# Optimization experiments

Measured on AMD Instinct MI355X. Metric: run time of the kernel, lower is better.

## Reference

```python
import jax, jax.numpy as jnp
import numpy as np
import math

B, S, D = 2, 2048, 1024
H = 16
HD = D // H
SPARSITY = 0.8


def setup_inputs() -> dict:
    key = jax.random.key(0)
    ks = jax.random.split(key, 5)
    scale = 1.0 / math.sqrt(D)
    return {
        "hidden_states": jax.random.normal(ks[0], (B, S, D), dtype=jnp.float32),
        "Wq": jax.random.normal(ks[1], (D, D), dtype=jnp.float32) * scale,
        "bq": jnp.zeros((D,), dtype=jnp.float32),
        "Wk": jax.random.normal(ks[2], (D, D), dtype=jnp.float32) * scale,
        "bk": jnp.zeros((D,), dtype=jnp.float32),
        "Wv": jax.random.normal(ks[3], (D, D), dtype=jnp.float32) * scale,
        "bv": jnp.zeros((D,), dtype=jnp.float32),
        "Wo": jax.random.normal(ks[4], (D, D), dtype=jnp.float32) * scale,
        "bo": jnp.zeros((D,), dtype=jnp.float32),
    }


def reference(hidden_states, Wq, bq, Wk, bk, Wv, bv, Wo, bo):
    b, s, d = hidden_states.shape
    # projections (torch Linear: x @ W.T + b), split heads -> [b, h, s, hd]
    def proj(W, bias):
        y = hidden_states @ W.T + bias
        return y.reshape(b, s, H, HD).transpose(0, 2, 1, 3)

    q = proj(Wq, bq)
    k = proj(Wk, bk)
    v = proj(Wv, bv)

    # scaled dot-product scores [b, h, s, s]
    attn = jnp.einsum("bhqd,bhkd->bhqk", q, k) / math.sqrt(HD)

    # top-k threshold per query row (k-th largest == sort-descending[k-1])
    kk = max(int(s * (1.0 - SPARSITY)), 1)
    thr = jax.lax.top_k(attn, kk)[0][..., kk - 1:kk]  # [b, h, s, 1]
    attn = attn + jnp.where(attn < thr, jnp.float32(-10000.0), jnp.float32(0.0))

    attn = jax.nn.softmax(attn, axis=-1)
    out = jnp.einsum("bhqk,bhkd->bhqd", attn, v)  # [b, h, s, hd]
    out = out.transpose(0, 2, 1, 3).reshape(b, s, d)
    return out @ Wo.T + bo
```

## Files before the change

### kernel.cpp

```cpp
#include <hip/hip_runtime.h>
#include <math.h>

#define S_LEN 2048
#define NH 16
#define HDIM 64
#define BATCH 2
#define BHC 32
#define KK 409
#define DMODEL 1024

typedef __attribute__((ext_vector_type(8))) short bf16x8;
typedef __attribute__((ext_vector_type(4))) float f32x4;

#define SC_STR 1032
#define P_STR  2056
#define T_STR  40

__device__ __forceinline__ unsigned f2ord(float f) {
    unsigned u = __float_as_uint(f);
    return (u & 0x80000000u) ? ~u : (u | 0x80000000u);
}
__device__ __forceinline__ float ord2f(unsigned v) {
    unsigned u = (v & 0x80000000u) ? (v & 0x7fffffffu) : ~v;
    return __uint_as_float(u);
}
__device__ __forceinline__ unsigned short f2bf(float f) {
    unsigned u = __float_as_uint(f);
    u += 0x7fffu + ((u >> 16) & 1u);
    return (unsigned short)(u >> 16);
}
__device__ __forceinline__ float bf2f(unsigned short h) {
    return __uint_as_float(((unsigned)h) << 16);
}

__global__ __launch_bounds__(256)
void split32(const float* __restrict__ in, unsigned short* __restrict__ hi,
             unsigned short* __restrict__ lo, int n4)
{
    const int i = blockIdx.x * 256 + threadIdx.x;
    if (i < n4) {
        const float4 v = ((const float4*)in)[i];
        ushort4 h, l;
        h.x = f2bf(v.x); l.x = f2bf(v.x - bf2f(h.x));
        h.y = f2bf(v.y); l.y = f2bf(v.y - bf2f(h.y));
        h.z = f2bf(v.z); l.z = f2bf(v.z - bf2f(h.z));
        h.w = f2bf(v.w); l.w = f2bf(v.w - bf2f(h.w));
        ((ushort4*)hi)[i] = h;
        ((ushort4*)lo)[i] = l;
    }
}

__global__ __launch_bounds__(256)
void gemm_mfma(const unsigned short* __restrict__ Ah, const unsigned short* __restrict__ Al,
               const unsigned short* __restrict__ Bh, const unsigned short* __restrict__ Bl,
               const float* __restrict__ bias, void* __restrict__ out0,
               void* __restrict__ out1, int mode)
{
    __shared__ __align__(16) unsigned short sAh[128 * T_STR];
    __shared__ __align__(16) unsigned short sAl[128 * T_STR];
    __shared__ __align__(16) unsigned short sBh[64 * T_STR];
    __shared__ __align__(16) unsigned short sBl[64 * T_STR];

    const int tid  = threadIdx.x;
    const int lane = tid & 63;
    const int w    = tid >> 6;
    const int q15  = lane & 15;
    const int quad = lane >> 4;
    const int n0b = blockIdx.x * 64;
    const int m0b = blockIdx.y * 128;
    const int wm = (w >> 1) * 64;
    const int wn = (w & 1) * 32;

    const int ar0 = tid >> 2, aks0 = (tid & 3) * 8;
    const int ar1 = (tid + 256) >> 2, aks1 = aks0;
    const int br = tid >> 2, bks = (tid & 3) * 8;

    const unsigned short* gAh0 = Ah + (size_t)(m0b + ar0) * 1024 + aks0;
    const unsigned short* gAh1 = Ah + (size_t)(m0b + ar1) * 1024 + aks1;
    const unsigned short* gAl0 = Al + (size_t)(m0b + ar0) * 1024 + aks0;
    const unsigned short* gAl1 = Al + (size_t)(m0b + ar1) * 1024 + aks1;
    const unsigned short* gBh = Bh + (size_t)(n0b + br) * 1024 + bks;
    const unsigned short* gBl = Bl + (size_t)(n0b + br) * 1024 + bks;

    f32x4 acc[4][2];
#pragma unroll
    for (int mt = 0; mt < 4; ++mt)
#pragma unroll
        for (int nt = 0; nt < 2; ++nt) acc[mt][nt] = (f32x4){0.f, 0.f, 0.f, 0.f};

#pragma unroll 1
    for (int k0 = 0; k0 < 1024; k0 += 32) {
        const bf16x8 vah0 = *(const bf16x8*)(gAh0 + k0);
        const bf16x8 vah1 = *(const bf16x8*)(gAh1 + k0);
        const bf16x8 val0 = *(const bf16x8*)(gAl0 + k0);
        const bf16x8 val1 = *(const bf16x8*)(gAl1 + k0);
        const bf16x8 vbh  = *(const bf16x8*)(gBh + k0);
        const bf16x8 vbl  = *(const bf16x8*)(gBl + k0);
        __syncthreads();
        *(bf16x8*)(sAh + ar0 * T_STR + aks0) = vah0;
        *(bf16x8*)(sAh + ar1 * T_STR + aks1) = vah1;
        *(bf16x8*)(sAl + ar0 * T_STR + aks0) = val0;
        *(bf16x8*)(sAl + ar1 * T_STR + aks1) = val1;
        *(bf16x8*)(sBh + br * T_STR + bks) = vbh;
        *(bf16x8*)(sBl + br * T_STR + bks) = vbl;
        __syncthreads();

        bf16x8 fbh[2], fbl[2];
#pragma unroll
        for (int nt = 0; nt < 2; ++nt) {
            fbh[nt] = *(const bf16x8*)(sBh + (wn + nt * 16 + q15) * T_STR + quad * 8);
            fbl[nt] = *(const bf16x8*)(sBl + (wn + nt * 16 + q15) * T_STR + quad * 8);
        }
#pragma unroll
        for (int mt = 0; mt < 4; ++mt) {
            const bf16x8 fah = *(const bf16x8*)(sAh + (wm + mt * 16 + q15) * T_STR + quad * 8);
            const bf16x8 fal = *(const bf16x8*)(sAl + (wm + mt * 16 + q15) * T_STR + quad * 8);
#pragma unroll
            for (int nt = 0; nt < 2; ++nt) {
                acc[mt][nt] = __builtin_amdgcn_mfma_f32_16x16x32_bf16(fah, fbh[nt], acc[mt][nt], 0, 0, 0);
                acc[mt][nt] = __builtin_amdgcn_mfma_f32_16x16x32_bf16(fah, fbl[nt], acc[mt][nt], 0, 0, 0);
                acc[mt][nt] = __builtin_amdgcn_mfma_f32_16x16x32_bf16(fal, fbh[nt], acc[mt][nt], 0, 0, 0);
            }
        }
    }

#pragma unroll
    for (int nt = 0; nt < 2; ++nt) {
        const int n = n0b + wn + nt * 16 + q15;
        const float bv = bias[n];
#pragma unroll
        for (int mt = 0; mt < 4; ++mt) {
            const int mb = m0b + wm + mt * 16 + quad * 4;
#pragma unroll
            for (int rg = 0; rg < 4; ++rg) {
                const int m = mb + rg;
                const float o = acc[mt][nt][rg] + bv;
                if (mode == 0) {
                    ((float*)out0)[(size_t)m * 1024 + n] = o;
                } else {
                    const int b = m >> 11, s = m & 2047;
                    const int h = n >> 6, hd = n & 63;
                    const size_t base = ((size_t)((b * NH + h) * S_LEN + s)) * HDIM + hd;
                    if (mode == 3) {
                        ((unsigned short*)out0)[base] = f2bf(o);
                    } else {
                        const unsigned short oh = f2bf(o);
                        ((unsigned short*)out0)[base] = oh;
                        ((unsigned short*)out1)[base] = f2bf(o - bf2f(oh));
                    }
                }
            }
        }
    }
}

__global__ __launch_bounds__(256)
void transpose_v16(const unsigned short* __restrict__ V, unsigned short* __restrict__ Vt)
{
    __shared__ unsigned short t[64][72];
    const int tid = threadIdx.x;
    const int s0 = blockIdx.x * 64;
    const int bh = blockIdx.y;
    const unsigned short* Vb = V + (size_t)bh * S_LEN * HDIM;
#pragma unroll
    for (int i = 0; i < 4; ++i) {
        const int f = tid + i * 256;
        const int s = f >> 4;
        const int hq = (f & 15) * 4;
        const ushort4 v = *(const ushort4*)(Vb + (size_t)(s0 + s) * HDIM + hq);
        t[s][hq + 0] = v.x; t[s][hq + 1] = v.y; t[s][hq + 2] = v.z; t[s][hq + 3] = v.w;
    }
    __syncthreads();
    unsigned short* Vtb = Vt + (size_t)bh * HDIM * S_LEN;
#pragma unroll
    for (int i = 0; i < 4; ++i) {
        const int f = tid + i * 256;
        const int hd = f >> 4;
        const int sq = (f & 15) * 4;
        ushort4 v;
        v.x = t[sq + 0][hd]; v.y = t[sq + 1][hd];
        v.z = t[sq + 2][hd]; v.w = t[sq + 3][hd];
        *(ushort4*)(Vtb + (size_t)hd * S_LEN + s0 + sq) = v;
    }
}

__device__ __forceinline__ unsigned radix_select(const unsigned* u)
{
    unsigned T = 0;
#pragma unroll 1
    for (int b = 31; b >= 0; --b) {
        const unsigned X = T | (1u << b);
        int cnt = 0;
#pragma unroll
        for (int i = 0; i < 32; ++i)
            cnt += __builtin_popcountll(__ballot(u[i] >= X));
        if (cnt >= KK) {
            T = X;
            if (cnt == KK) {
                unsigned mn = 0xffffffffu;
#pragma unroll
                for (int i = 0; i < 32; ++i) {
                    const unsigned v = (u[i] >= X) ? u[i] : 0xffffffffu;
                    mn = v < mn ? v : mn;
                }
#pragma unroll
                for (int off = 32; off >= 1; off >>= 1) {
                    const unsigned o = (unsigned)__shfl_xor((int)mn, off);
                    mn = o < mn ? o : mn;
                }
                return mn;
            }
        }
    }
    return T;
}

__global__ __launch_bounds__(512, 4)
void attn_kernel(const unsigned short* __restrict__ Qh, const unsigned short* __restrict__ Ql,
                 const unsigned short* __restrict__ Kh, const unsigned short* __restrict__ Kl,
                 const unsigned short* __restrict__ Vt,
                 unsigned short* __restrict__ AOh, unsigned short* __restrict__ AOl)
{
    extern __shared__ __align__(16) char smem[];
    float* sc = (float*)smem;
    unsigned short* P = (unsigned short*)smem;
    float* Opart = (float*)smem;

    const int tid  = threadIdx.x;
    const int lane = tid & 63;
    const int w    = tid >> 6;
    const int q15  = lane & 15;
    const int quad = lane >> 4;
    const int l5   = lane >> 5;
    const int l31  = lane & 31;

    const int blk = blockIdx.x;
    const int bh  = (blk & 7) * 4 + ((blk >> 3) & 3);
    const int q0  = (blk >> 5) * 16;

    const size_t qrow = ((size_t)bh * S_LEN + q0 + q15) * HDIM;
    const bf16x8 bqh0 = *(const bf16x8*)(Qh + qrow + quad * 8);
    const bf16x8 bqh1 = *(const bf16x8*)(Qh + qrow + 32 + quad * 8);
    const bf16x8 bql0 = *(const bf16x8*)(Ql + qrow + quad * 8);
    const bf16x8 bql1 = *(const bf16x8*)(Ql + qrow + 32 + quad * 8);

    const size_t kbase = (size_t)bh * S_LEN * HDIM;
    const int r0 = 2 * w, r1 = 2 * w + 1;
    unsigned u0[32], u1[32];

#pragma unroll 1
    for (int half = 0; half < 2; ++half) {
        f32x4 acc[8];
#pragma unroll 2
        for (int t = 0; t < 8; ++t) {
            const int key = w * 256 + half * 128 + t * 16 + q15;
            const unsigned short* kh = Kh + kbase + (size_t)key * HDIM + quad * 8;
            const unsigned short* kl = Kl + kbase + (size_t)key * HDIM + quad * 8;
            const bf16x8 akh0 = *(const bf16x8*)(kh);
            const bf16x8 akh1 = *(const bf16x8*)(kh + 32);
            const bf16x8 akl0 = *(const bf16x8*)(kl);
            const bf16x8 akl1 = *(const bf16x8*)(kl + 32);
            f32x4 c = {0.f, 0.f, 0.f, 0.f};
            c = __builtin_amdgcn_mfma_f32_16x16x32_bf16(akh0, bqh0, c, 0, 0, 0);
            c = __builtin_amdgcn_mfma_f32_16x16x32_bf16(akh1, bqh1, c, 0, 0, 0);
            c = __builtin_amdgcn_mfma_f32_16x16x32_bf16(akh0, bql0, c, 0, 0, 0);
            c = __builtin_amdgcn_mfma_f32_16x16x32_bf16(akh1, bql1, c, 0, 0, 0);
            c = __builtin_amdgcn_mfma_f32_16x16x32_bf16(akl0, bqh0, c, 0, 0, 0);
            c = __builtin_amdgcn_mfma_f32_16x16x32_bf16(akl1, bqh1, c, 0, 0, 0);
            acc[t] = c * 0.125f;
        }
        if (half) __syncthreads();
#pragma unroll
        for (int t = 0; t < 8; ++t)
            *(f32x4*)(sc + q15 * SC_STR + w * 128 + t * 16 + quad * 4) = acc[t];
        __syncthreads();
        unsigned* d0 = u0 + half * 16;
        unsigned* d1 = u1 + half * 16;
#pragma unroll
        for (int i = 0; i < 4; ++i) {
            const f32x4 v0 = *(const f32x4*)(sc + r0 * SC_STR + i * 256 + lane * 4);
            d0[4 * i + 0] = f2ord(v0[0]); d0[4 * i + 1] = f2ord(v0[1]);
            d0[4 * i + 2] = f2ord(v0[2]); d0[4 * i + 3] = f2ord(v0[3]);
            const f32x4 v1 = *(const f32x4*)(sc + r1 * SC_STR + i * 256 + lane * 4);
            d1[4 * i + 0] = f2ord(v1[0]); d1[4 * i + 1] = f2ord(v1[1]);
            d1[4 * i + 2] = f2ord(v1[2]); d1[4 * i + 3] = f2ord(v1[3]);
        }
    }
    __syncthreads();

    float invd[2];
#pragma unroll 1
    for (int rr = 0; rr < 2; ++rr) {
        const unsigned* u = rr ? u1 : u0;
        const int r = rr ? r1 : r0;
        const unsigned T = radix_select(u);
        unsigned umx = 0;
#pragma unroll
        for (int i = 0; i < 32; ++i) umx = u[i] > umx ? u[i] : umx;
#pragma unroll
        for (int off = 32; off >= 1; off >>= 1) {
            const unsigned o = (unsigned)__shfl_xor((int)umx, off);
            umx = o > umx ? o : umx;
        }
        const float mx = ord2f(umx);
        float lsum = 0.f;
        unsigned short* Pr = P + r * P_STR;
#pragma unroll
        for (int h = 0; h < 2; ++h) {
#pragma unroll
            for (int i = 0; i < 4; ++i) {
                const unsigned a0 = u[h * 16 + 4 * i + 0];
                const unsigned a1 = u[h * 16 + 4 * i + 1];
                const unsigned a2 = u[h * 16 + 4 * i + 2];
                const unsigned a3 = u[h * 16 + 4 * i + 3];
                const float e0 = (a0 >= T) ? __expf(ord2f(a0) - mx) : 0.f;
                const float e1 = (a1 >= T) ? __expf(ord2f(a1) - mx) : 0.f;
                const float e2 = (a2 >= T) ? __expf(ord2f(a2) - mx) : 0.f;
                const float e3 = (a3 >= T) ? __expf(ord2f(a3) - mx) : 0.f;
                ushort4 pk;
                pk.x = f2bf(e0); pk.y = f2bf(e1); pk.z = f2bf(e2); pk.w = f2bf(e3);
                const int key = (2 * i + l5) * 256 + h * 128 + l31 * 4;
                *(ushort4*)(Pr + key) = pk;
                lsum += e0 + e1 + e2 + e3;
            }
        }
#pragma unroll
        for (int off = 32; off >= 1; off >>= 1) lsum += __shfl_xor(lsum, off);
        invd[rr] = 1.f / lsum;
    }
    __syncthreads();

    {
        f32x4 oacc[4];
#pragma unroll
        for (int ht = 0; ht < 4; ++ht) oacc[ht] = (f32x4){0.f, 0.f, 0.f, 0.f};
        const size_t vtb = (size_t)bh * HDIM * S_LEN;
#pragma unroll 2
        for (int ks = 0; ks < 8; ++ks) {
            const int key0 = w * 256 + ks * 32 + quad * 8;
            const bf16x8 ap = *(const bf16x8*)(P + q15 * P_STR + key0);
#pragma unroll
            for (int ht = 0; ht < 4; ++ht) {
                const int hd = ht * 16 + q15;
                const bf16x8 bv = *(const bf16x8*)(Vt + vtb + (size_t)hd * S_LEN + key0);
                oacc[ht] = __builtin_amdgcn_mfma_f32_16x16x32_bf16(ap, bv, oacc[ht], 0, 0, 0);
            }
        }
        __syncthreads();
#pragma unroll
        for (int ht = 0; ht < 4; ++ht)
#pragma unroll
            for (int rg = 0; rg < 4; ++rg)
                Opart[w * 1024 + (quad * 4 + rg) * 64 + ht * 16 + q15] = oacc[ht][rg];
    }
    __syncthreads();

    {
        float s0 = 0.f, s1 = 0.f;
#pragma unroll
        for (int ww = 0; ww < 8; ++ww) {
            s0 += Opart[ww * 1024 + r0 * 64 + lane];
            s1 += Opart[ww * 1024 + r1 * 64 + lane];
        }
        const int b = bh >> 4, h = bh & 15;
        const float o0 = s0 * invd[0];
        const float o1 = s1 * invd[1];
        const size_t i0 = ((size_t)(b * S_LEN + q0 + r0)) * DMODEL + h * HDIM + lane;
        const size_t i1 = ((size_t)(b * S_LEN + q0 + r1)) * DMODEL + h * HDIM + lane;
        const unsigned short h0 = f2bf(o0), h1 = f2bf(o1);
        AOh[i0] = h0; AOl[i0] = f2bf(o0 - bf2f(h0));
        AOh[i1] = h1; AOl[i1] = f2bf(o1 - bf2f(h1));
    }
}

extern "C" void kernel_launch(void* const* d_in, const int* in_sizes, int n_in,
                              void* d_out, int out_size, void* d_ws, size_t ws_size,
                              hipStream_t stream)
{
    const float* X  = (const float*)d_in[0];
    const float* Wq = (const float*)d_in[1];
    const float* bq = (const float*)d_in[2];
    const float* Wk = (const float*)d_in[3];
    const float* bk = (const float*)d_in[4];
    const float* Wv = (const float*)d_in[5];
    const float* bv = (const float*)d_in[6];
    const float* Wo = (const float*)d_in[7];
    const float* bo = (const float*)d_in[8];

    char* p = (char*)d_ws;
    const size_t NEL = (size_t)BHC * S_LEN * HDIM;
    unsigned short* Q16h = (unsigned short*)p; p += NEL * 2;
    unsigned short* Q16l = (unsigned short*)p; p += NEL * 2;
    unsigned short* K16h = (unsigned short*)p; p += NEL * 2;
    unsigned short* K16l = (unsigned short*)p; p += NEL * 2;
    unsigned short* Vb16 = (unsigned short*)p; p += NEL * 2;
    unsigned short* Vt16 = (unsigned short*)p; p += NEL * 2;
    unsigned short* Xh   = (unsigned short*)p; p += NEL * 2;
    unsigned short* Xl   = (unsigned short*)p; p += NEL * 2;
    unsigned short* AOh  = (unsigned short*)p; p += NEL * 2;
    unsigned short* AOl  = (unsigned short*)p; p += NEL * 2;
    unsigned short* Wqh  = (unsigned short*)p; p += DMODEL * DMODEL * 2;
    unsigned short* Wql  = (unsigned short*)p; p += DMODEL * DMODEL * 2;
    unsigned short* Wkh  = (unsigned short*)p; p += DMODEL * DMODEL * 2;
    unsigned short* Wkl  = (unsigned short*)p; p += DMODEL * DMODEL * 2;
    unsigned short* Wvh  = (unsigned short*)p; p += DMODEL * DMODEL * 2;
    unsigned short* Wvl  = (unsigned short*)p; p += DMODEL * DMODEL * 2;
    unsigned short* Woh  = (unsigned short*)p; p += DMODEL * DMODEL * 2;
    unsigned short* Wol  = (unsigned short*)p; p += DMODEL * DMODEL * 2;

    const int attn_lds = 16 * SC_STR * 4;
    hipFuncSetAttribute((const void*)attn_kernel,
                        hipFuncAttributeMaxDynamicSharedMemorySize, attn_lds);

    const int X4 = (int)(NEL / 4);
    const int W4 = DMODEL * DMODEL / 4;

    split32<<<(X4 + 255) / 256, 256, 0, stream>>>(X,  Xh,  Xl,  X4);
    split32<<<(W4 + 255) / 256, 256, 0, stream>>>(Wq, Wqh, Wql, W4);
    split32<<<(W4 + 255) / 256, 256, 0, stream>>>(Wk, Wkh, Wkl, W4);
    split32<<<(W4 + 255) / 256, 256, 0, stream>>>(Wv, Wvh, Wvl, W4);
    split32<<<(W4 + 255) / 256, 256, 0, stream>>>(Wo, Woh, Wol, W4);

    const dim3 ggrid(16, 32, 1);
    gemm_mfma<<<ggrid, 256, 0, stream>>>(Xh, Xl, Wqh, Wql, bq, Q16h, Q16l, 2);
    gemm_mfma<<<ggrid, 256, 0, stream>>>(Xh, Xl, Wkh, Wkl, bk, K16h, K16l, 2);
    gemm_mfma<<<ggrid, 256, 0, stream>>>(Xh, Xl, Wvh, Wvl, bv, Vb16, nullptr, 3);
    transpose_v16<<<dim3(32, 32, 1), 256, 0, stream>>>(Vb16, Vt16);

    attn_kernel<<<4096, 512, attn_lds, stream>>>(Q16h, Q16l, K16h, K16l, Vt16, AOh, AOl);

    gemm_mfma<<<ggrid, 256, 0, stream>>>(AOh, AOl, Woh, Wol, bo, d_out, nullptr, 0);
}
```

Baseline: 856.6 us.

## Keep full score tile in LDS and reduce radix-select ballots via bit-sliced counts

```diff
diff --git a/kernel.cpp b/kernel.cpp
--- a/kernel.cpp
+++ b/kernel.cpp
@@ -12,8 +12,7 @@
 typedef __attribute__((ext_vector_type(8))) short bf16x8;
 typedef __attribute__((ext_vector_type(4))) float f32x4;
 
-#define SC_STR 1032
-#define P_STR  2056
+#define SSTR 2052
 #define T_STR  40
 
 __device__ __forceinline__ unsigned f2ord(float f) {
@@ -184,46 +183,24 @@
     }
 }
 
-__device__ __forceinline__ unsigned radix_select(const unsigned* u)
-{
-    unsigned T = 0;
-#pragma unroll 1
-    for (int b = 31; b >= 0; --b) {
-        const unsigned X = T | (1u << b);
-        int cnt = 0;
-#pragma unroll
-        for (int i = 0; i < 32; ++i)
-            cnt += __builtin_popcountll(__ballot(u[i] >= X));
-        if (cnt >= KK) {
-            T = X;
-            if (cnt == KK) {
-                unsigned mn = 0xffffffffu;
-#pragma unroll
-                for (int i = 0; i < 32; ++i) {
-                    const unsigned v = (u[i] >= X) ? u[i] : 0xffffffffu;
-                    mn = v < mn ? v : mn;
-                }
-#pragma unroll
-                for (int off = 32; off >= 1; off >>= 1) {
-                    const unsigned o = (unsigned)__shfl_xor((int)mn, off);
-                    mn = o < mn ? o : mn;
-                }
-                return mn;
-            }
-        }
-    }
-    return T;
-}
-
-__global__ __launch_bounds__(512, 4)
+__device__ __forceinline__ bf16x8 pack_hi8(const uint4 a0, const uint4 a1)
+{
+    union { unsigned u[4]; bf16x8 v; } c;
+    c.u[0] = (a0.x >> 16) | (a0.y & 0xffff0000u);
+    c.u[1] = (a0.z >> 16) | (a0.w & 0xffff0000u);
+    c.u[2] = (a1.x >> 16) | (a1.y & 0xffff0000u);
+    c.u[3] = (a1.z >> 16) | (a1.w & 0xffff0000u);
+    return c.v;
+}
+
+__global__ __launch_bounds__(512, 2)
 void attn_kernel(const unsigned short* __restrict__ Qh, const unsigned short* __restrict__ Ql,
                  const unsigned short* __restrict__ Kh, const unsigned short* __restrict__ Kl,
                  const unsigned short* __restrict__ Vt,
                  unsigned short* __restrict__ AOh, unsigned short* __restrict__ AOl)
 {
     extern __shared__ __align__(16) char smem[];
-    float* sc = (float*)smem;
-    unsigned short* P = (unsigned short*)smem;
+    unsigned* S = (unsigned*)smem;
     float* Opart = (float*)smem;
 
     const int tid  = threadIdx.x;
@@ -231,8 +208,6 @@
     const int w    = tid >> 6;
     const int q15  = lane & 15;
     const int quad = lane >> 4;
-    const int l5   = lane >> 5;
-    const int l31  = lane & 31;
 
     const int blk = blockIdx.x;
     const int bh  = (blk & 7) * 4 + ((blk >> 3) & 3);
@@ -245,84 +220,107 @@
     const bf16x8 bql1 = *(const bf16x8*)(Ql + qrow + 32 + quad * 8);
 
     const size_t kbase = (size_t)bh * S_LEN * HDIM;
-    const int r0 = 2 * w, r1 = 2 * w + 1;
-    unsigned u0[32], u1[32];
-
-#pragma unroll 1
-    for (int half = 0; half < 2; ++half) {
-        f32x4 acc[8];
-#pragma unroll 2
-        for (int t = 0; t < 8; ++t) {
-            const int key = w * 256 + half * 128 + t * 16 + q15;
-            const unsigned short* kh = Kh + kbase + (size_t)key * HDIM + quad * 8;
-            const unsigned short* kl = Kl + kbase + (size_t)key * HDIM + quad * 8;
-            const bf16x8 akh0 = *(const bf16x8*)(kh);
-            const bf16x8 akh1 = *(const bf16x8*)(kh + 32);
-            const bf16x8 akl0 = *(const bf16x8*)(kl);
-            const bf16x8 akl1 = *(const bf16x8*)(kl + 32);
-            f32x4 c = {0.f, 0.f, 0.f, 0.f};
-            c = __builtin_amdgcn_mfma_f32_16x16x32_bf16(akh0, bqh0, c, 0, 0, 0);
-            c = __builtin_amdgcn_mfma_f32_16x16x32_bf16(akh1, bqh1, c, 0, 0, 0);
-            c = __builtin_amdgcn_mfma_f32_16x16x32_bf16(akh0, bql0, c, 0, 0, 0);
-            c = __builtin_amdgcn_mfma_f32_16x16x32_bf16(akh1, bql1, c, 0, 0, 0);
-            c = __builtin_amdgcn_mfma_f32_16x16x32_bf16(akl0, bqh0, c, 0, 0, 0);
-            c = __builtin_amdgcn_mfma_f32_16x16x32_bf16(akl1, bqh1, c, 0, 0, 0);
-            acc[t] = c * 0.125f;
-        }
-        if (half) __syncthreads();
-#pragma unroll
-        for (int t = 0; t < 8; ++t)
-            *(f32x4*)(sc + q15 * SC_STR + w * 128 + t * 16 + quad * 4) = acc[t];
-        __syncthreads();
-        unsigned* d0 = u0 + half * 16;
-        unsigned* d1 = u1 + half * 16;
-#pragma unroll
-        for (int i = 0; i < 4; ++i) {
-            const f32x4 v0 = *(const f32x4*)(sc + r0 * SC_STR + i * 256 + lane * 4);
-            d0[4 * i + 0] = f2ord(v0[0]); d0[4 * i + 1] = f2ord(v0[1]);
-            d0[4 * i + 2] = f2ord(v0[2]); d0[4 * i + 3] = f2ord(v0[3]);
-            const f32x4 v1 = *(const f32x4*)(sc + r1 * SC_STR + i * 256 + lane * 4);
-            d1[4 * i + 0] = f2ord(v1[0]); d1[4 * i + 1] = f2ord(v1[1]);
-            d1[4 * i + 2] = f2ord(v1[2]); d1[4 * i + 3] = f2ord(v1[3]);
-        }
+
+#pragma unroll 4
+    for (int t = 0; t < 16; ++t) {
+        const int key = w * 256 + t * 16 + q15;
+        const unsigned short* kh = Kh + kbase + (size_t)key * HDIM + quad * 8;
+        const unsigned short* kl = Kl + kbase + (size_t)key * HDIM + quad * 8;
+        const bf16x8 akh0 = *(const bf16x8*)(kh);
+        const bf16x8 akh1 = *(const bf16x8*)(kh + 32);
+        const bf16x8 akl0 = *(const bf16x8*)(kl);
+        const bf16x8 akl1 = *(const bf16x8*)(kl + 32);
+        f32x4 c = {0.f, 0.f, 0.f, 0.f};
+        c = __builtin_amdgcn_mfma_f32_16x16x32_bf16(akh0, bqh0, c, 0, 0, 0);
+        c = __builtin_amdgcn_mfma_f32_16x16x32_bf16(akh1, bqh1, c, 0, 0, 0);
+        c = __builtin_amdgcn_mfma_f32_16x16x32_bf16(akh0, bql0, c, 0, 0, 0);
+        c = __builtin_amdgcn_mfma_f32_16x16x32_bf16(akh1, bql1, c, 0, 0, 0);
+        c = __builtin_amdgcn_mfma_f32_16x16x32_bf16(akl0, bqh0, c, 0, 0, 0);
+        c = __builtin_amdgcn_mfma_f32_16x16x32_bf16(akl1, bqh1, c, 0, 0, 0);
+        c = c * 0.125f;
+        uint4 o;
+        o.x = f2ord(c[0]); o.y = f2ord(c[1]); o.z = f2ord(c[2]); o.w = f2ord(c[3]);
+        *(uint4*)(S + q15 * SSTR + w * 256 + t * 16 + quad * 4) = o;
     }
     __syncthreads();
 
     float invd[2];
-#pragma unroll 1
+    const int r0 = 2 * w;
+#pragma unroll
     for (int rr = 0; rr < 2; ++rr) {
-        const unsigned* u = rr ? u1 : u0;
-        const int r = rr ? r1 : r0;
-        const unsigned T = radix_select(u);
-        unsigned umx = 0;
-#pragma unroll
-        for (int i = 0; i < 32; ++i) umx = u[i] > umx ? u[i] : umx;
+        const int r = r0 + rr;
+        unsigned* R = S + r * SSTR;
+
+        uint4 va[8];
+#pragma unroll
+        for (int i = 0; i < 8; ++i) va[i] = *(const uint4*)(R + i * 256 + lane * 4);
+
+        unsigned umx = 0u;
+#pragma unroll
+        for (int i = 0; i < 8; ++i) {
+            umx = va[i].x > umx ? va[i].x : umx;
+            umx = va[i].y > umx ? va[i].y : umx;
+            umx = va[i].z > umx ? va[i].z : umx;
+            umx = va[i].w > umx ? va[i].w : umx;
+        }
 #pragma unroll
         for (int off = 32; off >= 1; off >>= 1) {
             const unsigned o = (unsigned)__shfl_xor((int)umx, off);
             umx = o > umx ? o : umx;
         }
         const float mx = ord2f(umx);
+
+        unsigned T = 0u;
+#pragma unroll 1
+        for (int b = 31; b >= 0; --b) {
+            const unsigned X = T | (1u << b);
+            int c = 0;
+#pragma unroll
+            for (int i = 0; i < 8; ++i) {
+                c += (va[i].x >= X) + (va[i].y >= X) + (va[i].z >= X) + (va[i].w >= X);
+            }
+            int cnt = 0;
+#pragma unroll
+            for (int bb = 0; bb < 6; ++bb)
+                cnt += (int)(__builtin_popcountll(__ballot((c >> bb) & 1)) << bb);
+            if (cnt >= KK) {
+                T = X;
+                if (cnt == KK) {
+                    unsigned mn = 0xffffffffu;
+#pragma unroll
+                    for (int i = 0; i < 8; ++i) {
+                        unsigned v;
+                        v = va[i].x >= X ? va[i].x : 0xffffffffu; mn = v < mn ? v : mn;
+                        v = va[i].y >= X ? va[i].y : 0xffffffffu; mn = v < mn ? v : mn;
+                        v = va[i].z >= X ? va[i].z : 0xffffffffu; mn = v < mn ? v : mn;
+                        v = va[i].w >= X ? va[i].w : 0xffffffffu; mn = v < mn ? v : mn;
+                    }
+#pragma unroll
+                    for (int off = 32; off >= 1; off >>= 1) {
+                        const unsigned o = (unsigned)__shfl_xor((int)mn, off);
+                        mn = o < mn ? o : mn;
+                    }
+                    T = mn;
+                    break;
+                }
+            }
+        }
+
         float lsum = 0.f;
-        unsigned short* Pr = P + r * P_STR;
-#pragma unroll
-        for (int h = 0; h < 2; ++h) {
-#pragma unroll
-            for (int i = 0; i < 4; ++i) {
-                const unsigned a0 = u[h * 16 + 4 * i + 0];
-                const unsigned a1 = u[h * 16 + 4 * i + 1];
-                const unsigned a2 = u[h * 16 + 4 * i + 2];
-                const unsigned a3 = u[h * 16 + 4 * i + 3];
-                const float e0 = (a0 >= T) ? __expf(ord2f(a0) - mx) : 0.f;
-                const float e1 = (a1 >= T) ? __expf(ord2f(a1) - mx) : 0.f;
-                const float e2 = (a2 >= T) ? __expf(ord2f(a2) - mx) : 0.f;
-                const float e3 = (a3 >= T) ? __expf(ord2f(a3) - mx) : 0.f;
-                ushort4 pk;
-                pk.x = f2bf(e0); pk.y = f2bf(e1); pk.z = f2bf(e2); pk.w = f2bf(e3);
-                const int key = (2 * i + l5) * 256 + h * 128 + l31 * 4;
-                *(ushort4*)(Pr + key) = pk;
-                lsum += e0 + e1 + e2 + e3;
-            }
+#pragma unroll
+        for (int i = 0; i < 8; ++i) {
+            const uint4 v = va[i];
+            const float e0 = (v.x >= T) ? __expf(ord2f(v.x) - mx) : 0.f;
+            const float e1 = (v.y >= T) ? __expf(ord2f(v.y) - mx) : 0.f;
+            const float e2 = (v.z >= T) ? __expf(ord2f(v.z) - mx) : 0.f;
+            const float e3 = (v.w >= T) ? __expf(ord2f(v.w) - mx) : 0.f;
+            uint4 pw;
+            pw.x = ((unsigned)f2bf(e0)) << 16;
+            pw.y = ((unsigned)f2bf(e1)) << 16;
+            pw.z = ((unsigned)f2bf(e2)) << 16;
+            pw.w = ((unsigned)f2bf(e3)) << 16;
+            *(uint4*)(R + i * 256 + lane * 4) = pw;
+            lsum += e0 + e1 + e2 + e3;
         }
 #pragma unroll
         for (int off = 32; off >= 1; off >>= 1) lsum += __shfl_xor(lsum, off);
@@ -335,10 +333,13 @@
 #pragma unroll
         for (int ht = 0; ht < 4; ++ht) oacc[ht] = (f32x4){0.f, 0.f, 0.f, 0.f};
         const size_t vtb = (size_t)bh * HDIM * S_LEN;
+        const unsigned* Srow = S + q15 * SSTR;
 #pragma unroll 2
         for (int ks = 0; ks < 8; ++ks) {
             const int key0 = w * 256 + ks * 32 + quad * 8;
-            const bf16x8 ap = *(const bf16x8*)(P + q15 * P_STR + key0);
+            const uint4 a0 = *(const uint4*)(Srow + key0);
+            const uint4 a1 = *(const uint4*)(Srow + key0 + 4);
+            const bf16x8 ap = pack_hi8(a0, a1);
 #pragma unroll
             for (int ht = 0; ht < 4; ++ht) {
                 const int hd = ht * 16 + q15;
@@ -356,6 +357,7 @@
     __syncthreads();
 
     {
+        const int r1 = r0 + 1;
         float s0 = 0.f, s1 = 0.f;
 #pragma unroll
         for (int ww = 0; ww < 8; ++ww) {
@@ -408,7 +410,7 @@
     unsigned short* Woh  = (unsigned short*)p; p += DMODEL * DMODEL * 2;
     unsigned short* Wol  = (unsigned short*)p; p += DMODEL * DMODEL * 2;
 
-    const int attn_lds = 16 * SC_STR * 4;
+    const int attn_lds = 16 * SSTR * 4;
     hipFuncSetAttribute((const void*)attn_kernel,
                         hipFuncAttributeMaxDynamicSharedMemorySize, attn_lds);
 
```

Result: slower. 938.1 us (+9.5%).
